# Optimization experiments

Measured on AMD Instinct MI355X. Metric: run time of the kernel, lower is better.

The kernel has to match this reference:

```python
import jax, jax.numpy as jnp
import numpy as np

B, S, D = 4, 2048, 256
H = 8
KD = D  # keras MHA key_dim = input_shape[-1] -> per-head dim equals D
EPS = 1e-5


def layer_norm(x, gamma, beta):
    mu = jnp.mean(x, axis=-1, keepdims=True)
    var = jnp.var(x, axis=-1, keepdims=True)
    return (x - mu) * jax.lax.rsqrt(var + EPS) * gamma + beta


def setup_inputs() -> dict:
    key = jax.random.key(0)
    ks = jax.random.split(key, 12)
    scale = 1.0 / np.sqrt(D)
    inp = {
        "input_query": jax.random.normal(ks[0], (B, S, D), jnp.float32),
        "key": jax.random.normal(ks[1], (B, S, D), jnp.float32),
        "value": jax.random.normal(ks[2], (B, S, D), jnp.float32),
        # LayerNorm params (3 separate norms)
        "gq": jnp.ones((D,), jnp.float32), "bq_ln": jnp.zeros((D,), jnp.float32),
        "gk": jnp.ones((D,), jnp.float32), "bk_ln": jnp.zeros((D,), jnp.float32),
        "gv": jnp.ones((D,), jnp.float32), "bv_ln": jnp.zeros((D,), jnp.float32),
        # MHA projection weights: [D, H, KD] for q/k/v, [H, KD, D] for output
        "Wq": jax.random.normal(ks[3], (D, H, KD), jnp.float32) * scale,
        "bq": jnp.zeros((H, KD), jnp.float32),
        "Wk": jax.random.normal(ks[4], (D, H, KD), jnp.float32) * scale,
        "bk": jnp.zeros((H, KD), jnp.float32),
        "Wv": jax.random.normal(ks[5], (D, H, KD), jnp.float32) * scale,
        "bv": jnp.zeros((H, KD), jnp.float32),
        "Wo": jax.random.normal(ks[6], (H, KD, D), jnp.float32) * scale,
        "bo": jnp.zeros((D,), jnp.float32),
    }
    return inp


def reference(input_query, key, value, gq, bq_ln, gk, bk_ln, gv, bv_ln,
              Wq, bq, Wk, bk, Wv, bv, Wo, bo):
    # pre-LN on each stream
    q_in = layer_norm(input_query, gq, bq_ln)
    k_in = layer_norm(key, gk, bk_ln)
    v_in = layer_norm(value, gv, bv_ln)

    # projections -> [B, S, H, KD]
    q = jnp.einsum('bsd,dhk->bshk', q_in, Wq) + bq
    k = jnp.einsum('bsd,dhk->bshk', k_in, Wk) + bk
    v = jnp.einsum('bsd,dhk->bshk', v_in, Wv) + bv

    # scaled dot-product attention (keras scales query by 1/sqrt(key_dim))
    q = q * (1.0 / np.sqrt(KD)).astype(np.float32)
    scores = jnp.einsum('bqhk,bshk->bhqs', q, k)  # [B, H, Sq, Sk]
    probs = jax.nn.softmax(scores, axis=-1)
    # dropout = 0.0 (inference)
    attn = jnp.einsum('bhqs,bshk->bqhk', probs, v)
    out = jnp.einsum('bqhk,hkd->bqd', attn, Wo) + bo

    return input_query + out
```

## Files before the change

### kernel.cpp

```cpp
#include <hip/hip_runtime.h>

using bf16x8 = __attribute__((ext_vector_type(8))) __bf16;
using f32x4  = __attribute__((ext_vector_type(4))) float;
using f32x16 = __attribute__((ext_vector_type(16))) float;
typedef unsigned short u16;
typedef const __attribute__((address_space(1))) void* gas_p;
typedef __attribute__((address_space(3))) void* las_p;

__device__ __forceinline__ u16 f2bf(float f) {
  union { float f; unsigned u; } v; v.f = f;
  unsigned r = v.u + 0x7fffu + ((v.u >> 16) & 1u);
  return (u16)(r >> 16);
}

__device__ __forceinline__ unsigned pkbf(float a, float b) {
  unsigned r;
  asm("v_cvt_pk_bf16_f32 %0, %1, %2" : "=v"(r) : "v"(a), "v"(b));
  return r;
}

__device__ __forceinline__ void gload16(const void* g, void* l) {
  __builtin_amdgcn_global_load_lds((gas_p)g, (las_p)l, 16, 0, 0);
}

#define MFMA(a, b, c)   __builtin_amdgcn_mfma_f32_16x16x32_bf16((a), (b), (c), 0, 0, 0)
#define MFMA32(a, b, c) __builtin_amdgcn_mfma_f32_32x32x16_bf16((a), (b), (c), 0, 0, 0)

__global__ __launch_bounds__(256) void transpose_conv(
    const float* __restrict__ Wq, const float* __restrict__ Wk,
    const float* __restrict__ Wv, const float* __restrict__ Wo,
    u16* __restrict__ wqt, u16* __restrict__ wkt,
    u16* __restrict__ wvt, u16* __restrict__ wot)
{
  int z = blockIdx.y;
  const float* src = (z == 0) ? Wq : (z == 1) ? Wk : (z == 2) ? Wv : Wo;
  u16* dst = (z == 0) ? wqt : (z == 1) ? wkt : (z == 2) ? wvt : wot;
  int C = (z < 3) ? 2048 : 256;
  int R = (z < 3) ? 256 : 2048;
  int TC = C >> 5;
  int tc = blockIdx.x % TC, tr = blockIdx.x / TC;
  __shared__ float tile[32][33];
  int j = threadIdx.x & 31, i0 = threadIdx.x >> 5;
#pragma unroll
  for (int p = 0; p < 4; p++)
    tile[i0 + p * 8][j] = src[(tr * 32 + i0 + p * 8) * C + tc * 32 + j];
  __syncthreads();
#pragma unroll
  for (int p = 0; p < 4; p++)
    dst[(tc * 32 + i0 + p * 8) * R + tr * 32 + j] = f2bf(tile[j][i0 + p * 8]);
}

__global__ __launch_bounds__(256) void ln3_kernel(
    const float* __restrict__ xq, const float* __restrict__ xk, const float* __restrict__ xv,
    const float* __restrict__ gq, const float* __restrict__ bq,
    const float* __restrict__ gk, const float* __restrict__ bk,
    const float* __restrict__ gv, const float* __restrict__ bv,
    u16* __restrict__ oq, u16* __restrict__ ok, u16* __restrict__ ov)
{
  int z = blockIdx.y;
  const float* x = (z == 0) ? xq : (z == 1) ? xk : xv;
  const float* g = (z == 0) ? gq : (z == 1) ? gk : gv;
  const float* be = (z == 0) ? bq : (z == 1) ? bk : bv;
  u16* o = (z == 0) ? oq : (z == 1) ? ok : ov;
  int w = threadIdx.x >> 6, l = threadIdx.x & 63;
  int row = blockIdx.x * 4 + w;
  float4 x4 = *(const float4*)(x + row * 256 + l * 4);
  float s = x4.x + x4.y + x4.z + x4.w;
  float sq = x4.x * x4.x + x4.y * x4.y + x4.z * x4.z + x4.w * x4.w;
#pragma unroll
  for (int mm = 1; mm < 64; mm <<= 1) { s += __shfl_xor(s, mm); sq += __shfl_xor(sq, mm); }
  float mu = s * (1.f / 256.f);
  float var = sq * (1.f / 256.f) - mu * mu;
  float rs = rsqrtf(var + 1e-5f);
  float4 g4 = *(const float4*)(g + l * 4);
  float4 b4 = *(const float4*)(be + l * 4);
  ushort4 o4;
  o4.x = f2bf((x4.x - mu) * rs * g4.x + b4.x);
  o4.y = f2bf((x4.y - mu) * rs * g4.y + b4.y);
  o4.z = f2bf((x4.z - mu) * rs * g4.z + b4.z);
  o4.w = f2bf((x4.w - mu) * rs * g4.w + b4.w);
  *(ushort4*)(o + row * 256 + l * 4) = o4;
}

__global__ __launch_bounds__(256) void proj_gemm(
    const u16* __restrict__ qn, const u16* __restrict__ kn, const u16* __restrict__ vn,
    const u16* __restrict__ wqt, const u16* __restrict__ wkt, const u16* __restrict__ wvt,
    const float* __restrict__ bq, const float* __restrict__ bk, const float* __restrict__ bv,
    u16* __restrict__ qo, u16* __restrict__ ko, u16* __restrict__ vo)
{
  __shared__ u16 As[128 * 64];
  __shared__ u16 Bs[128 * 64];
  int z = blockIdx.z;
  const u16* A  = (z == 0) ? qn : (z == 1) ? kn : vn;
  const u16* Bt = (z == 0) ? wqt : (z == 1) ? wkt : wvt;
  const float* bias = (z == 0) ? bq : (z == 1) ? bk : bv;
  u16* Co = (z == 0) ? qo : (z == 1) ? ko : vo;
  float scale = (z == 0) ? 0.0625f : 1.0f;

  int i0 = blockIdx.x * 128, n0 = blockIdx.y * 128;
  int tid = threadIdx.x, w = tid >> 6, l = tid & 63;
  int wr = w >> 1, wc = w & 1, l15 = l & 15, qv = l >> 4;

  f32x4 acc[4][4] = {};

  for (int k0 = 0; k0 < 256; k0 += 64) {
    __syncthreads();
#pragma unroll
    for (int j = 0; j < 4; j++) {
      int c = (w * 4 + j) * 64 + l;
      int row = c >> 3, co = (c & 7) * 8;
      gload16(A + (i0 + row) * 256 + k0 + co, (char*)As + (w * 4 + j) * 1024);
      gload16(Bt + (n0 + row) * 256 + k0 + co, (char*)Bs + (w * 4 + j) * 1024);
    }
    __syncthreads();
#pragma unroll
    for (int kk = 0; kk < 2; kk++) {
      bf16x8 a[4], bfr[4];
#pragma unroll
      for (int m = 0; m < 4; m++)
        a[m] = *(const bf16x8*)(As + (wr * 64 + m * 16 + l15) * 64 + kk * 32 + qv * 8);
#pragma unroll
      for (int n = 0; n < 4; n++)
        bfr[n] = *(const bf16x8*)(Bs + (wc * 64 + n * 16 + l15) * 64 + kk * 32 + qv * 8);
#pragma unroll
      for (int m = 0; m < 4; m++)
#pragma unroll
        for (int n = 0; n < 4; n++) acc[m][n] = MFMA(a[m], bfr[n], acc[m][n]);
    }
  }

  if (z == 2) {
#pragma unroll
    for (int n = 0; n < 4; n++) {
      int col = n0 + wc * 64 + n * 16 + l15;
      float bc = bias[col];
      int h = col >> 8, kd = col & 255;
#pragma unroll
      for (int m = 0; m < 4; m++) {
        int row0 = i0 + wr * 64 + m * 16 + qv * 4;
        int bb = row0 >> 11, ss = row0 & 2047;
        ushort4 o4;
        o4.x = f2bf(acc[m][n][0] + bc);
        o4.y = f2bf(acc[m][n][1] + bc);
        o4.z = f2bf(acc[m][n][2] + bc);
        o4.w = f2bf(acc[m][n][3] + bc);
        *(ushort4*)(Co + ((size_t)(bb * 8 + h) * 256 + kd) * 2048 + ss) = o4;
      }
    }
  } else {
#pragma unroll
    for (int n = 0; n < 4; n++) {
      int col = n0 + wc * 64 + n * 16 + l15;
      float bc = bias[col];
      int h = col >> 8, kd = col & 255;
#pragma unroll
      for (int m = 0; m < 4; m++) {
#pragma unroll
        for (int r = 0; r < 4; r++) {
          int row = i0 + wr * 64 + m * 16 + qv * 4 + r;
          int bb = row >> 11, ss = row & 2047;
          Co[((bb * 8 + h) * 2048 + ss) * 256 + kd] = f2bf((acc[m][n][r] + bc) * scale);
        }
      }
    }
  }
}

__global__ __launch_bounds__(512, 2) void flash_attn(
    const u16* __restrict__ q, const u16* __restrict__ k,
    const u16* __restrict__ vt, u16* __restrict__ o)
{
  __shared__ char lds[131072];
  int f = blockIdx.x;
  int qt = f >> 5;
  int bh = (f & 7) | (((f >> 3) & 3) << 3);
  int b = bh >> 3, hh = bh & 7;
  int tid = threadIdx.x, w = tid >> 6, l = tid & 63;
  int l31 = l & 31, h = l >> 5;

  const u16* Q = q + (size_t)(bh * 2048 + qt * 256 + w * 32) * 256;
  const u16* K = k + (size_t)bh * 2048 * 256;
  const u16* V = vt + (size_t)bh * 256 * 2048;

  bf16x8 qf[16];
#pragma unroll
  for (int dt = 0; dt < 16; dt++)
    qf[dt] = *(const bf16x8*)(Q + l31 * 256 + dt * 16 + h * 8);

  f32x16 oacc[8] = {};
  float m_ = -1e30f, lsum = 0.f;

  auto stage = [&](int t, char* base) {
#pragma unroll
    for (int j = 0; j < 4; j++) {
      int c = w * 4 + j;
      int off = c * 1024 + l * 16;
      {
        int r = off >> 9, ps = l & 31;
        gload16(K + (size_t)(t * 64 + r) * 256 + ((ps ^ (r & 31)) << 3), base + off);
      }
      {
        int r = off >> 8, ps = l & 15;
        int lsl = ps ^ (r & 15);
        int d = r * 2 + (lsl >> 3);
        gload16(V + (size_t)d * 2048 + t * 64 + ((lsl & 7) << 3), base + 32768 + off);
      }
    }
  };

  stage(0, lds);
  __syncthreads();

  for (int t = 0; t < 32; t++) {
    char* cur = lds + (size_t)(t & 1) * 65536;
    char* nxt = lds + (size_t)((t + 1) & 1) * 65536;
    if (t + 1 < 32) stage(t + 1, nxt);

    f32x16 p0 = {}, p1 = {};
    __builtin_amdgcn_s_setprio(1);
#pragma unroll
    for (int dt = 0; dt < 16; dt++) {
      int sl = ((dt * 2 + h) ^ l31) << 4;
      bf16x8 kf0 = *(const bf16x8*)(cur + l31 * 512 + sl);
      bf16x8 kf1 = *(const bf16x8*)(cur + (32 + l31) * 512 + sl);
      p0 = MFMA32(kf0, qf[dt], p0);
      p1 = MFMA32(kf1, qf[dt], p1);
    }
    __builtin_amdgcn_s_setprio(0);

    float n0 = fmaxf(fmaxf(p0[0], p0[1]), fmaxf(p0[2], p0[3]));
    float n1 = fmaxf(fmaxf(p0[4], p0[5]), fmaxf(p0[6], p0[7]));
    float n2 = fmaxf(fmaxf(p0[8], p0[9]), fmaxf(p0[10], p0[11]));
    float n3 = fmaxf(fmaxf(p0[12], p0[13]), fmaxf(p0[14], p0[15]));
    float n4 = fmaxf(fmaxf(p1[0], p1[1]), fmaxf(p1[2], p1[3]));
    float n5 = fmaxf(fmaxf(p1[4], p1[5]), fmaxf(p1[6], p1[7]));
    float n6 = fmaxf(fmaxf(p1[8], p1[9]), fmaxf(p1[10], p1[11]));
    float n7 = fmaxf(fmaxf(p1[12], p1[13]), fmaxf(p1[14], p1[15]));
    float mt = fmaxf(fmaxf(fmaxf(n0, n1), fmaxf(n2, n3)),
                     fmaxf(fmaxf(n4, n5), fmaxf(n6, n7)));
    mt = fmaxf(mt, __shfl_xor(mt, 32));
    if (__any(mt > m_ + 8.0f)) {
      float mn = fmaxf(m_, mt);
      float fsc = __expf(m_ - mn);
      lsum *= fsc;
#pragma unroll
      for (int dt = 0; dt < 8; dt++)
#pragma unroll
        for (int i = 0; i < 16; i++) oacc[dt][i] *= fsc;
      m_ = mn;
    }
#pragma unroll
    for (int i = 0; i < 16; i++) { p0[i] = __expf(p0[i] - m_); lsum += p0[i]; }
#pragma unroll
    for (int i = 0; i < 16; i++) { p1[i] = __expf(p1[i] - m_); lsum += p1[i]; }

    unsigned pw[16];
#pragma unroll
    for (int i = 0; i < 8; i++) pw[i] = pkbf(p0[2 * i], p0[2 * i + 1]);
#pragma unroll
    for (int i = 0; i < 8; i++) pw[8 + i] = pkbf(p1[2 * i], p1[2 * i + 1]);

#pragma unroll
    for (int kt = 0; kt < 4; kt++) {
      unsigned x0 = __shfl_xor(pw[4 * kt + 0], 32);
      unsigned x1 = __shfl_xor(pw[4 * kt + 1], 32);
      unsigned x2 = __shfl_xor(pw[4 * kt + 2], 32);
      unsigned x3 = __shfl_xor(pw[4 * kt + 3], 32);
      union { unsigned u[4]; bf16x8 v; } pa;
      pa.u[0] = h ? x2 : pw[4 * kt + 0];
      pa.u[1] = h ? x3 : pw[4 * kt + 1];
      pa.u[2] = h ? pw[4 * kt + 2] : x0;
      pa.u[3] = h ? pw[4 * kt + 3] : x1;
      __builtin_amdgcn_s_setprio(1);
#pragma unroll
      for (int dt = 0; dt < 8; dt++) {
        int d = dt * 32 + l31;
        int r = d >> 1;
        int lsl = (d & 1) * 8 + kt * 2 + h;
        bf16x8 vf = *(const bf16x8*)(cur + 32768 + r * 256 + ((lsl ^ (r & 15)) << 4));
        oacc[dt] = MFMA32(vf, pa.v, oacc[dt]);
      }
      __builtin_amdgcn_s_setprio(0);
    }

    asm volatile("s_waitcnt vmcnt(0)" ::: "memory");
    __syncthreads();
  }

  __syncthreads();
  float inv = 1.0f / (lsum + __shfl_xor(lsum, 32));
  char* wbase = (char*)lds + w * 8192;
  int qr15 = l31 & 15;
#pragma unroll
  for (int ph = 0; ph < 2; ph++) {
    if ((l31 >> 4) == ph) {
#pragma unroll
      for (int dt = 0; dt < 8; dt++) {
#pragma unroll
        for (int rg = 0; rg < 4; rg++) {
          uint2 uu;
          uu.x = pkbf(oacc[dt][rg * 4 + 0] * inv, oacc[dt][rg * 4 + 1] * inv);
          uu.y = pkbf(oacc[dt][rg * 4 + 2] * inv, oacc[dt][rg * 4 + 3] * inv);
          *(uint2*)(wbase + qr15 * 512 + ((dt * 64 + rg * 16) ^ (qr15 << 4)) + h * 8) = uu;
        }
      }
    }
    asm volatile("s_waitcnt lgkmcnt(0)" ::: "memory");
    __builtin_amdgcn_sched_barrier(0);
#pragma unroll
    for (int c = 0; c < 8; c++) {
      int qr = c * 2 + h;
      uint4 vv = *(const uint4*)(wbase + qr * 512 + ((l31 ^ qr) << 4));
      int s = qt * 256 + w * 32 + ph * 16 + qr;
      *(uint4*)((char*)o + (size_t)(b * 2048 + s) * 4096 + hh * 512 + l31 * 16) = vv;
    }
    asm volatile("s_waitcnt lgkmcnt(0)" ::: "memory");
  }
}

__global__ __launch_bounds__(256) void out_gemm(
    const u16* __restrict__ A, const u16* __restrict__ Bt,
    const float* __restrict__ bo, const float* __restrict__ resid,
    float* __restrict__ out)
{
  __shared__ u16 As[128 * 64];
  __shared__ u16 Bs[64 * 64];
  int i0 = blockIdx.x * 128, n0 = blockIdx.y * 64;
  int tid = threadIdx.x, w = tid >> 6, l = tid & 63, l15 = l & 15, qv = l >> 4;

  f32x4 acc[2][4] = {};

  for (int k0 = 0; k0 < 2048; k0 += 64) {
    __syncthreads();
#pragma unroll
    for (int j = 0; j < 4; j++) {
      int c = (w * 4 + j) * 64 + l;
      int row = c >> 3, co = (c & 7) * 8;
      gload16(A + (i0 + row) * 2048 + k0 + co, (char*)As + (w * 4 + j) * 1024);
    }
#pragma unroll
    for (int j = 0; j < 2; j++) {
      int c = (w * 2 + j) * 64 + l;
      int row = c >> 3, co = (c & 7) * 8;
      gload16(Bt + (n0 + row) * 2048 + k0 + co, (char*)Bs + (w * 2 + j) * 1024);
    }
    __syncthreads();
#pragma unroll
    for (int kk = 0; kk < 2; kk++) {
      bf16x8 a[2], bfr[4];
#pragma unroll
      for (int m = 0; m < 2; m++)
        a[m] = *(const bf16x8*)(As + (w * 32 + m * 16 + l15) * 64 + kk * 32 + qv * 8);
#pragma unroll
      for (int n = 0; n < 4; n++)
        bfr[n] = *(const bf16x8*)(Bs + (n * 16 + l15) * 64 + kk * 32 + qv * 8);
#pragma unroll
      for (int m = 0; m < 2; m++)
#pragma unroll
        for (int n = 0; n < 4; n++) acc[m][n] = MFMA(a[m], bfr[n], acc[m][n]);
    }
  }

#pragma unroll
  for (int n = 0; n < 4; n++) {
    int col = n0 + n * 16 + l15;
    float bc = bo[col];
#pragma unroll
    for (int m = 0; m < 2; m++)
#pragma unroll
      for (int r = 0; r < 4; r++) {
        int row = i0 + w * 32 + m * 16 + qv * 4 + r;
        out[row * 256 + col] = acc[m][n][r] + bc + resid[row * 256 + col];
      }
  }
}

extern "C" void kernel_launch(void* const* d_in, const int* in_sizes, int n_in,
                              void* d_out, int out_size, void* d_ws, size_t ws_size,
                              hipStream_t stream)
{
  const float* inq  = (const float*)d_in[0];
  const float* key  = (const float*)d_in[1];
  const float* val  = (const float*)d_in[2];
  const float* gq   = (const float*)d_in[3];
  const float* bqln = (const float*)d_in[4];
  const float* gk   = (const float*)d_in[5];
  const float* bkln = (const float*)d_in[6];
  const float* gv   = (const float*)d_in[7];
  const float* bvln = (const float*)d_in[8];
  const float* Wq   = (const float*)d_in[9];
  const float* bq   = (const float*)d_in[10];
  const float* Wk   = (const float*)d_in[11];
  const float* bk   = (const float*)d_in[12];
  const float* Wv   = (const float*)d_in[13];
  const float* bv   = (const float*)d_in[14];
  const float* Wo   = (const float*)d_in[15];
  const float* bo   = (const float*)d_in[16];

  char* ws = (char*)d_ws;
  const size_t MB = 1ull << 20;
  u16* wqt = (u16*)(ws + 0 * MB);
  u16* wkt = (u16*)(ws + 1 * MB);
  u16* wvt = (u16*)(ws + 2 * MB);
  u16* wot = (u16*)(ws + 3 * MB);
  u16* qn  = (u16*)(ws + 4 * MB);
  u16* kn  = (u16*)(ws + 8 * MB);
  u16* vn  = (u16*)(ws + 12 * MB);
  u16* qws = (u16*)(ws + 16 * MB);
  u16* kws = (u16*)(ws + 48 * MB);
  u16* attn = (u16*)(ws + 80 * MB);
  u16* vtw = (u16*)(ws + 112 * MB);

  transpose_conv<<<dim3(512, 4), 256, 0, stream>>>(Wq, Wk, Wv, Wo, wqt, wkt, wvt, wot);
  ln3_kernel<<<dim3(2048, 3), 256, 0, stream>>>(inq, key, val, gq, bqln, gk, bkln, gv, bvln,
                                                qn, kn, vn);
  proj_gemm<<<dim3(64, 16, 3), 256, 0, stream>>>(qn, kn, vn, wqt, wkt, wvt, bq, bk, bv,
                                                 qws, kws, vtw);
  flash_attn<<<256, 512, 0, stream>>>(qws, kws, vtw, attn);
  out_gemm<<<dim3(64, 4), 256, 0, stream>>>(attn, wot, bo, inq, (float*)d_out);
}
```

Baseline: 267.3 us.

## Shrink flash-attention tiles to 128 queries and 32-key blocks with 4 waves

Flash attention now uses 256-thread blocks covering 128 query rows (down from 512 threads and 256 rows) and streams K/V in 32-key tiles instead of 64-key tiles. LDS drops from 128KB to 64KB and the grid doubles to 512 blocks, with a new block-to-(batch,head,qtile) mapping. The aim is more blocks and higher occupancy across the CUs. The cost is twice as many loop iterations, each with its own barrier and staging overhead, and less K/V reuse per block. The swizzled LDS layouts for K and V are reworked to match the new tile sizes, and the redundant barrier before the epilogue is removed.

```diff
diff --git a/kernel.cpp b/kernel.cpp
--- a/kernel.cpp
+++ b/kernel.cpp
@@ -166,19 +166,20 @@
   }
 }
 
-__global__ __launch_bounds__(512, 2) void flash_attn(
+__global__ __launch_bounds__(256, 2) void flash_attn(
     const u16* __restrict__ q, const u16* __restrict__ k,
     const u16* __restrict__ vt, u16* __restrict__ o)
 {
-  __shared__ char lds[131072];
+  __shared__ char lds[65536];
   int f = blockIdx.x;
-  int qt = f >> 5;
-  int bh = (f & 7) | (((f >> 3) & 3) << 3);
+  int slot = f >> 3;
+  int bh = (f & 7) * 4 + (slot & 3);
+  int qt = slot >> 2;
   int b = bh >> 3, hh = bh & 7;
   int tid = threadIdx.x, w = tid >> 6, l = tid & 63;
   int l31 = l & 31, h = l >> 5;
 
-  const u16* Q = q + (size_t)(bh * 2048 + qt * 256 + w * 32) * 256;
+  const u16* Q = q + (size_t)(bh * 2048 + qt * 128 + w * 32) * 256;
   const u16* K = k + (size_t)bh * 2048 * 256;
   const u16* V = vt + (size_t)bh * 256 * 2048;
 
@@ -196,14 +197,14 @@
       int c = w * 4 + j;
       int off = c * 1024 + l * 16;
       {
-        int r = off >> 9, ps = l & 31;
-        gload16(K + (size_t)(t * 64 + r) * 256 + ((ps ^ (r & 31)) << 3), base + off);
+        int r = off >> 9, ps = (off >> 4) & 31;
+        gload16(K + (size_t)(t * 32 + r) * 256 + ((ps ^ r) << 3), base + off);
       }
       {
-        int r = off >> 8, ps = l & 15;
-        int lsl = ps ^ (r & 15);
-        int d = r * 2 + (lsl >> 3);
-        gload16(V + (size_t)d * 2048 + t * 64 + ((lsl & 7) << 3), base + 32768 + off);
+        int r = off >> 8, g = (off >> 4) & 15;
+        int gg = g ^ (r & 15);
+        int d = r * 4 + (gg >> 2), s0 = (gg & 3) * 8;
+        gload16(V + (size_t)d * 2048 + t * 32 + s0, base + 16384 + off);
       }
     }
   };
@@ -211,33 +212,25 @@
   stage(0, lds);
   __syncthreads();
 
-  for (int t = 0; t < 32; t++) {
-    char* cur = lds + (size_t)(t & 1) * 65536;
-    char* nxt = lds + (size_t)((t + 1) & 1) * 65536;
-    if (t + 1 < 32) stage(t + 1, nxt);
-
-    f32x16 p0 = {}, p1 = {};
+  for (int t = 0; t < 64; t++) {
+    char* cur = lds + (size_t)(t & 1) * 32768;
+    char* nxt = lds + (size_t)((t + 1) & 1) * 32768;
+    if (t + 1 < 64) stage(t + 1, nxt);
+
+    f32x16 p = {};
     __builtin_amdgcn_s_setprio(1);
 #pragma unroll
     for (int dt = 0; dt < 16; dt++) {
-      int sl = ((dt * 2 + h) ^ l31) << 4;
-      bf16x8 kf0 = *(const bf16x8*)(cur + l31 * 512 + sl);
-      bf16x8 kf1 = *(const bf16x8*)(cur + (32 + l31) * 512 + sl);
-      p0 = MFMA32(kf0, qf[dt], p0);
-      p1 = MFMA32(kf1, qf[dt], p1);
+      bf16x8 kf = *(const bf16x8*)(cur + l31 * 512 + (((dt * 2 + h) ^ l31) << 4));
+      p = MFMA32(kf, qf[dt], p);
     }
     __builtin_amdgcn_s_setprio(0);
 
-    float n0 = fmaxf(fmaxf(p0[0], p0[1]), fmaxf(p0[2], p0[3]));
-    float n1 = fmaxf(fmaxf(p0[4], p0[5]), fmaxf(p0[6], p0[7]));
-    float n2 = fmaxf(fmaxf(p0[8], p0[9]), fmaxf(p0[10], p0[11]));
-    float n3 = fmaxf(fmaxf(p0[12], p0[13]), fmaxf(p0[14], p0[15]));
-    float n4 = fmaxf(fmaxf(p1[0], p1[1]), fmaxf(p1[2], p1[3]));
-    float n5 = fmaxf(fmaxf(p1[4], p1[5]), fmaxf(p1[6], p1[7]));
-    float n6 = fmaxf(fmaxf(p1[8], p1[9]), fmaxf(p1[10], p1[11]));
-    float n7 = fmaxf(fmaxf(p1[12], p1[13]), fmaxf(p1[14], p1[15]));
-    float mt = fmaxf(fmaxf(fmaxf(n0, n1), fmaxf(n2, n3)),
-                     fmaxf(fmaxf(n4, n5), fmaxf(n6, n7)));
+    float n0 = fmaxf(fmaxf(p[0], p[1]), fmaxf(p[2], p[3]));
+    float n1 = fmaxf(fmaxf(p[4], p[5]), fmaxf(p[6], p[7]));
+    float n2 = fmaxf(fmaxf(p[8], p[9]), fmaxf(p[10], p[11]));
+    float n3 = fmaxf(fmaxf(p[12], p[13]), fmaxf(p[14], p[15]));
+    float mt = fmaxf(fmaxf(n0, n1), fmaxf(n2, n3));
     mt = fmaxf(mt, __shfl_xor(mt, 32));
     if (__any(mt > m_ + 8.0f)) {
       float mn = fmaxf(m_, mt);
@@ -250,18 +243,14 @@
       m_ = mn;
     }
 #pragma unroll
-    for (int i = 0; i < 16; i++) { p0[i] = __expf(p0[i] - m_); lsum += p0[i]; }
-#pragma unroll
-    for (int i = 0; i < 16; i++) { p1[i] = __expf(p1[i] - m_); lsum += p1[i]; }
-
-    unsigned pw[16];
-#pragma unroll
-    for (int i = 0; i < 8; i++) pw[i] = pkbf(p0[2 * i], p0[2 * i + 1]);
-#pragma unroll
-    for (int i = 0; i < 8; i++) pw[8 + i] = pkbf(p1[2 * i], p1[2 * i + 1]);
-
-#pragma unroll
-    for (int kt = 0; kt < 4; kt++) {
+    for (int i = 0; i < 16; i++) { p[i] = __expf(p[i] - m_); lsum += p[i]; }
+
+    unsigned pw[8];
+#pragma unroll
+    for (int i = 0; i < 8; i++) pw[i] = pkbf(p[2 * i], p[2 * i + 1]);
+
+#pragma unroll
+    for (int kt = 0; kt < 2; kt++) {
       unsigned x0 = __shfl_xor(pw[4 * kt + 0], 32);
       unsigned x1 = __shfl_xor(pw[4 * kt + 1], 32);
       unsigned x2 = __shfl_xor(pw[4 * kt + 2], 32);
@@ -275,9 +264,9 @@
 #pragma unroll
       for (int dt = 0; dt < 8; dt++) {
         int d = dt * 32 + l31;
-        int r = d >> 1;
-        int lsl = (d & 1) * 8 + kt * 2 + h;
-        bf16x8 vf = *(const bf16x8*)(cur + 32768 + r * 256 + ((lsl ^ (r & 15)) << 4));
+        int r = d >> 2;
+        int gg = (d & 3) * 4 + kt * 2 + h;
+        bf16x8 vf = *(const bf16x8*)(cur + 16384 + r * 256 + ((gg ^ (r & 15)) << 4));
         oacc[dt] = MFMA32(vf, pa.v, oacc[dt]);
       }
       __builtin_amdgcn_s_setprio(0);
@@ -287,7 +276,6 @@
     __syncthreads();
   }
 
-  __syncthreads();
   float inv = 1.0f / (lsum + __shfl_xor(lsum, 32));
   char* wbase = (char*)lds + w * 8192;
   int qr15 = l31 & 15;
@@ -311,7 +299,7 @@
     for (int c = 0; c < 8; c++) {
       int qr = c * 2 + h;
       uint4 vv = *(const uint4*)(wbase + qr * 512 + ((l31 ^ qr) << 4));
-      int s = qt * 256 + w * 32 + ph * 16 + qr;
+      int s = qt * 128 + w * 32 + ph * 16 + qr;
       *(uint4*)((char*)o + (size_t)(b * 2048 + s) * 4096 + hh * 512 + l31 * 16) = vv;
     }
     asm volatile("s_waitcnt lgkmcnt(0)" ::: "memory");
@@ -416,6 +404,6 @@
                                                 qn, kn, vn);
   proj_gemm<<<dim3(64, 16, 3), 256, 0, stream>>>(qn, kn, vn, wqt, wkt, wvt, bq, bk, bv,
                                                  qws, kws, vtw);
-  flash_attn<<<256, 512, 0, stream>>>(qws, kws, vtw, attn);
+  flash_attn<<<512, 256, 0, stream>>>(qws, kws, vtw, attn);
   out_gemm<<<dim3(64, 4), 256, 0, stream>>>(attn, wot, bo, inq, (float*)d_out);
 }
```

Measured after the change: 313.1 us. 17.2% more time.

## Split attention tile into halves and use exp2 with log2e-folded query scale

Applied to the files above, without the earlier changes.

Folds log2(e) into the query projection scale so softmax can use the native v_exp_f32 (exp2) instead of __expf, dropping a multiply per element. The 64-key tile is also processed as two 32-key halves: QK for the first half, then its softmax and PV, then the second half, so softmax VALU work can interleave with the other half's MFMAs. The running max can now be rescaled twice per tile, which may add rescale work. The threshold for lazy rescaling is scaled to match the new log2 domain.

```diff
diff --git a/kernel.cpp b/kernel.cpp
--- a/kernel.cpp
+++ b/kernel.cpp
@@ -7,6 +7,8 @@
 typedef const __attribute__((address_space(1))) void* gas_p;
 typedef __attribute__((address_space(3))) void* las_p;
 
+#define LOG2E 1.4426950408889634f
+
 __device__ __forceinline__ u16 f2bf(float f) {
   union { float f; unsigned u; } v; v.f = f;
   unsigned r = v.u + 0x7fffu + ((v.u >> 16) & 1u);
@@ -16,6 +18,12 @@
 __device__ __forceinline__ unsigned pkbf(float a, float b) {
   unsigned r;
   asm("v_cvt_pk_bf16_f32 %0, %1, %2" : "=v"(r) : "v"(a), "v"(b));
+  return r;
+}
+
+__device__ __forceinline__ float exp2v(float x) {
+  float r;
+  asm("v_exp_f32 %0, %1" : "=v"(r) : "v"(x));
   return r;
 }
 
@@ -95,7 +103,7 @@
   const u16* Bt = (z == 0) ? wqt : (z == 1) ? wkt : wvt;
   const float* bias = (z == 0) ? bq : (z == 1) ? bk : bv;
   u16* Co = (z == 0) ? qo : (z == 1) ? ko : vo;
-  float scale = (z == 0) ? 0.0625f : 1.0f;
+  float scale = (z == 0) ? 0.0625f * LOG2E : 1.0f;
 
   int i0 = blockIdx.x * 128, n0 = blockIdx.y * 128;
   int tid = threadIdx.x, w = tid >> 6, l = tid & 63;
@@ -208,40 +216,16 @@
     }
   };
 
-  stage(0, lds);
-  __syncthreads();
-
-  for (int t = 0; t < 32; t++) {
-    char* cur = lds + (size_t)(t & 1) * 65536;
-    char* nxt = lds + (size_t)((t + 1) & 1) * 65536;
-    if (t + 1 < 32) stage(t + 1, nxt);
-
-    f32x16 p0 = {}, p1 = {};
-    __builtin_amdgcn_s_setprio(1);
-#pragma unroll
-    for (int dt = 0; dt < 16; dt++) {
-      int sl = ((dt * 2 + h) ^ l31) << 4;
-      bf16x8 kf0 = *(const bf16x8*)(cur + l31 * 512 + sl);
-      bf16x8 kf1 = *(const bf16x8*)(cur + (32 + l31) * 512 + sl);
-      p0 = MFMA32(kf0, qf[dt], p0);
-      p1 = MFMA32(kf1, qf[dt], p1);
-    }
-    __builtin_amdgcn_s_setprio(0);
-
-    float n0 = fmaxf(fmaxf(p0[0], p0[1]), fmaxf(p0[2], p0[3]));
-    float n1 = fmaxf(fmaxf(p0[4], p0[5]), fmaxf(p0[6], p0[7]));
-    float n2 = fmaxf(fmaxf(p0[8], p0[9]), fmaxf(p0[10], p0[11]));
-    float n3 = fmaxf(fmaxf(p0[12], p0[13]), fmaxf(p0[14], p0[15]));
-    float n4 = fmaxf(fmaxf(p1[0], p1[1]), fmaxf(p1[2], p1[3]));
-    float n5 = fmaxf(fmaxf(p1[4], p1[5]), fmaxf(p1[6], p1[7]));
-    float n6 = fmaxf(fmaxf(p1[8], p1[9]), fmaxf(p1[10], p1[11]));
-    float n7 = fmaxf(fmaxf(p1[12], p1[13]), fmaxf(p1[14], p1[15]));
-    float mt = fmaxf(fmaxf(fmaxf(n0, n1), fmaxf(n2, n3)),
-                     fmaxf(fmaxf(n4, n5), fmaxf(n6, n7)));
+  auto softmax_half = [&](f32x16& p, unsigned* pw) {
+    float n0 = fmaxf(fmaxf(p[0], p[1]), fmaxf(p[2], p[3]));
+    float n1 = fmaxf(fmaxf(p[4], p[5]), fmaxf(p[6], p[7]));
+    float n2 = fmaxf(fmaxf(p[8], p[9]), fmaxf(p[10], p[11]));
+    float n3 = fmaxf(fmaxf(p[12], p[13]), fmaxf(p[14], p[15]));
+    float mt = fmaxf(fmaxf(n0, n1), fmaxf(n2, n3));
     mt = fmaxf(mt, __shfl_xor(mt, 32));
-    if (__any(mt > m_ + 8.0f)) {
+    if (__any(mt > m_ + 8.0f * LOG2E)) {
       float mn = fmaxf(m_, mt);
-      float fsc = __expf(m_ - mn);
+      float fsc = exp2v(m_ - mn);
       lsum *= fsc;
 #pragma unroll
       for (int dt = 0; dt < 8; dt++)
@@ -250,27 +234,24 @@
       m_ = mn;
     }
 #pragma unroll
-    for (int i = 0; i < 16; i++) { p0[i] = __expf(p0[i] - m_); lsum += p0[i]; }
-#pragma unroll
-    for (int i = 0; i < 16; i++) { p1[i] = __expf(p1[i] - m_); lsum += p1[i]; }
-
-    unsigned pw[16];
-#pragma unroll
-    for (int i = 0; i < 8; i++) pw[i] = pkbf(p0[2 * i], p0[2 * i + 1]);
-#pragma unroll
-    for (int i = 0; i < 8; i++) pw[8 + i] = pkbf(p1[2 * i], p1[2 * i + 1]);
-
-#pragma unroll
-    for (int kt = 0; kt < 4; kt++) {
-      unsigned x0 = __shfl_xor(pw[4 * kt + 0], 32);
-      unsigned x1 = __shfl_xor(pw[4 * kt + 1], 32);
-      unsigned x2 = __shfl_xor(pw[4 * kt + 2], 32);
-      unsigned x3 = __shfl_xor(pw[4 * kt + 3], 32);
+    for (int i = 0; i < 16; i++) { p[i] = exp2v(p[i] - m_); lsum += p[i]; }
+#pragma unroll
+    for (int i = 0; i < 8; i++) pw[i] = pkbf(p[2 * i], p[2 * i + 1]);
+  };
+
+  auto pv_half = [&](const unsigned* pw, int hf, const char* cur) {
+#pragma unroll
+    for (int ktl = 0; ktl < 2; ktl++) {
+      int kt = hf * 2 + ktl;
+      unsigned x0 = __shfl_xor(pw[4 * ktl + 0], 32);
+      unsigned x1 = __shfl_xor(pw[4 * ktl + 1], 32);
+      unsigned x2 = __shfl_xor(pw[4 * ktl + 2], 32);
+      unsigned x3 = __shfl_xor(pw[4 * ktl + 3], 32);
       union { unsigned u[4]; bf16x8 v; } pa;
-      pa.u[0] = h ? x2 : pw[4 * kt + 0];
-      pa.u[1] = h ? x3 : pw[4 * kt + 1];
-      pa.u[2] = h ? pw[4 * kt + 2] : x0;
-      pa.u[3] = h ? pw[4 * kt + 3] : x1;
+      pa.u[0] = h ? x2 : pw[4 * ktl + 0];
+      pa.u[1] = h ? x3 : pw[4 * ktl + 1];
+      pa.u[2] = h ? pw[4 * ktl + 2] : x0;
+      pa.u[3] = h ? pw[4 * ktl + 3] : x1;
       __builtin_amdgcn_s_setprio(1);
 #pragma unroll
       for (int dt = 0; dt < 8; dt++) {
@@ -282,6 +263,37 @@
       }
       __builtin_amdgcn_s_setprio(0);
     }
+  };
+
+  stage(0, lds);
+  __syncthreads();
+
+  for (int t = 0; t < 32; t++) {
+    char* cur = lds + (size_t)(t & 1) * 65536;
+    char* nxt = lds + (size_t)((t + 1) & 1) * 65536;
+    if (t + 1 < 32) stage(t + 1, nxt);
+
+    f32x16 p0 = {}, p1 = {};
+    unsigned pw0[8], pw1[8];
+    __builtin_amdgcn_s_setprio(1);
+#pragma unroll
+    for (int dt = 0; dt < 16; dt++) {
+      int sl = ((dt * 2 + h) ^ l31) << 4;
+      bf16x8 kf0 = *(const bf16x8*)(cur + l31 * 512 + sl);
+      p0 = MFMA32(kf0, qf[dt], p0);
+    }
+#pragma unroll
+    for (int dt = 0; dt < 16; dt++) {
+      int sl = ((dt * 2 + h) ^ l31) << 4;
+      bf16x8 kf1 = *(const bf16x8*)(cur + (32 + l31) * 512 + sl);
+      p1 = MFMA32(kf1, qf[dt], p1);
+    }
+    __builtin_amdgcn_s_setprio(0);
+
+    softmax_half(p0, pw0);
+    pv_half(pw0, 0, cur);
+    softmax_half(p1, pw1);
+    pv_half(pw1, 1, cur);
 
     asm volatile("s_waitcnt vmcnt(0)" ::: "memory");
     __syncthreads();
```

New measurement: 334.6 us. 1.25x slower.

## Use FP8 for P·V in flash attention with exp2 softmax

Applied to the files above, without the earlier changes.

The V projection is now written as FP8 in a permuted layout, and the attention probabilities are packed to FP8, so the P·V product uses 32x32x16 fp8 MFMAs instead of bf16. This halves V staging traffic and the LDS footprint. Log2e is folded into the Q scale so the softmax can use raw v_exp_f32, and permlane32_swap replaces the xor-32 shuffles. Precision drops noticeably for both P and V, and the rescale threshold is tightened.

```diff
diff --git a/kernel.cpp b/kernel.cpp
--- a/kernel.cpp
+++ b/kernel.cpp
@@ -3,9 +3,12 @@
 using bf16x8 = __attribute__((ext_vector_type(8))) __bf16;
 using f32x4  = __attribute__((ext_vector_type(4))) float;
 using f32x16 = __attribute__((ext_vector_type(16))) float;
+using uint2v = __attribute__((ext_vector_type(2))) unsigned;
 typedef unsigned short u16;
 typedef const __attribute__((address_space(1))) void* gas_p;
 typedef __attribute__((address_space(3))) void* las_p;
+
+#define LOG2E 1.4426950408889634f
 
 __device__ __forceinline__ u16 f2bf(float f) {
   union { float f; unsigned u; } v; v.f = f;
@@ -19,12 +22,29 @@
   return r;
 }
 
+__device__ __forceinline__ float exp2v(float x) {
+  float r;
+  asm("v_exp_f32 %0, %1" : "=v"(r) : "v"(x));
+  return r;
+}
+
+__device__ __forceinline__ unsigned pk_fp8x4(float a, float b, float c, float d) {
+  int w = __builtin_amdgcn_cvt_pk_fp8_f32(a, b, 0, false);
+  w = __builtin_amdgcn_cvt_pk_fp8_f32(c, d, w, true);
+  return (unsigned)w;
+}
+
+__device__ __forceinline__ uint2v swap32(unsigned a, unsigned b) {
+  return __builtin_amdgcn_permlane32_swap(a, b, false, false);
+}
+
 __device__ __forceinline__ void gload16(const void* g, void* l) {
   __builtin_amdgcn_global_load_lds((gas_p)g, (las_p)l, 16, 0, 0);
 }
 
 #define MFMA(a, b, c)   __builtin_amdgcn_mfma_f32_16x16x32_bf16((a), (b), (c), 0, 0, 0)
 #define MFMA32(a, b, c) __builtin_amdgcn_mfma_f32_32x32x16_bf16((a), (b), (c), 0, 0, 0)
+#define MFMA8(a, b, c)  __builtin_amdgcn_mfma_f32_32x32x16_fp8_fp8((a), (b), (c), 0, 0, 0)
 
 __global__ __launch_bounds__(256) void transpose_conv(
     const float* __restrict__ Wq, const float* __restrict__ Wk,
@@ -86,7 +106,7 @@
     const u16* __restrict__ qn, const u16* __restrict__ kn, const u16* __restrict__ vn,
     const u16* __restrict__ wqt, const u16* __restrict__ wkt, const u16* __restrict__ wvt,
     const float* __restrict__ bq, const float* __restrict__ bk, const float* __restrict__ bv,
-    u16* __restrict__ qo, u16* __restrict__ ko, u16* __restrict__ vo)
+    u16* __restrict__ qo, u16* __restrict__ ko, unsigned char* __restrict__ vo)
 {
   __shared__ u16 As[128 * 64];
   __shared__ u16 Bs[128 * 64];
@@ -94,8 +114,7 @@
   const u16* A  = (z == 0) ? qn : (z == 1) ? kn : vn;
   const u16* Bt = (z == 0) ? wqt : (z == 1) ? wkt : wvt;
   const float* bias = (z == 0) ? bq : (z == 1) ? bk : bv;
-  u16* Co = (z == 0) ? qo : (z == 1) ? ko : vo;
-  float scale = (z == 0) ? 0.0625f : 1.0f;
+  float scale = (z == 0) ? 0.0625f * LOG2E : 1.0f;
 
   int i0 = blockIdx.x * 128, n0 = blockIdx.y * 128;
   int tid = threadIdx.x, w = tid >> 6, l = tid & 63;
@@ -134,32 +153,31 @@
     for (int n = 0; n < 4; n++) {
       int col = n0 + wc * 64 + n * 16 + l15;
       float bc = bias[col];
-      int h = col >> 8, kd = col & 255;
+      int hd = col >> 8, kd = col & 255;
 #pragma unroll
       for (int m = 0; m < 4; m++) {
         int row0 = i0 + wr * 64 + m * 16 + qv * 4;
         int bb = row0 >> 11, ss = row0 & 2047;
-        ushort4 o4;
-        o4.x = f2bf(acc[m][n][0] + bc);
-        o4.y = f2bf(acc[m][n][1] + bc);
-        o4.z = f2bf(acc[m][n][2] + bc);
-        o4.w = f2bf(acc[m][n][3] + bc);
-        *(ushort4*)(Co + ((size_t)(bb * 8 + h) * 256 + kd) * 2048 + ss) = o4;
+        unsigned wv = pk_fp8x4(acc[m][n][0] + bc, acc[m][n][1] + bc,
+                               acc[m][n][2] + bc, acc[m][n][3] + bc);
+        int pos = (ss & ~63) | (((ss >> 3) & 3) << 4) | (((ss >> 5) & 1) << 3) | (ss & 7);
+        *(unsigned*)(vo + ((size_t)(bb * 8 + hd) * 256 + kd) * 2048 + pos) = wv;
       }
     }
   } else {
+    u16* Co = (z == 0) ? qo : ko;
 #pragma unroll
     for (int n = 0; n < 4; n++) {
       int col = n0 + wc * 64 + n * 16 + l15;
       float bc = bias[col];
-      int h = col >> 8, kd = col & 255;
+      int hd = col >> 8, kd = col & 255;
 #pragma unroll
       for (int m = 0; m < 4; m++) {
 #pragma unroll
         for (int r = 0; r < 4; r++) {
           int row = i0 + wr * 64 + m * 16 + qv * 4 + r;
           int bb = row >> 11, ss = row & 2047;
-          Co[((bb * 8 + h) * 2048 + ss) * 256 + kd] = f2bf((acc[m][n][r] + bc) * scale);
+          Co[((bb * 8 + hd) * 2048 + ss) * 256 + kd] = f2bf((acc[m][n][r] + bc) * scale);
         }
       }
     }
@@ -168,9 +186,9 @@
 
 __global__ __launch_bounds__(512, 2) void flash_attn(
     const u16* __restrict__ q, const u16* __restrict__ k,
-    const u16* __restrict__ vt, u16* __restrict__ o)
-{
-  __shared__ char lds[131072];
+    const unsigned char* __restrict__ vt, u16* __restrict__ o)
+{
+  __shared__ char lds[98304];
   int f = blockIdx.x;
   int qt = f >> 5;
   int bh = (f & 7) | (((f >> 3) & 3) << 3);
@@ -180,7 +198,7 @@
 
   const u16* Q = q + (size_t)(bh * 2048 + qt * 256 + w * 32) * 256;
   const u16* K = k + (size_t)bh * 2048 * 256;
-  const u16* V = vt + (size_t)bh * 256 * 2048;
+  const unsigned char* V = vt + (size_t)bh * 256 * 2048;
 
   bf16x8 qf[16];
 #pragma unroll
@@ -195,16 +213,17 @@
     for (int j = 0; j < 4; j++) {
       int c = w * 4 + j;
       int off = c * 1024 + l * 16;
-      {
-        int r = off >> 9, ps = l & 31;
-        gload16(K + (size_t)(t * 64 + r) * 256 + ((ps ^ (r & 31)) << 3), base + off);
-      }
-      {
-        int r = off >> 8, ps = l & 15;
-        int lsl = ps ^ (r & 15);
-        int d = r * 2 + (lsl >> 3);
-        gload16(V + (size_t)d * 2048 + t * 64 + ((lsl & 7) << 3), base + 32768 + off);
-      }
+      int r = off >> 9, ps = l & 31;
+      gload16(K + (size_t)(t * 64 + r) * 256 + ((ps ^ (r & 31)) << 3), base + off);
+    }
+#pragma unroll
+    for (int j = 0; j < 2; j++) {
+      int c = w * 2 + j;
+      int off = c * 1024 + l * 16;
+      int r = off >> 8, pg = (off >> 4) & 15;
+      int g = pg ^ (r & 15);
+      int d = r + 64 * (g >> 2), sc = g & 3;
+      gload16(V + (size_t)d * 2048 + t * 64 + sc * 16, base + 32768 + off);
     }
   };
 
@@ -212,8 +231,8 @@
   __syncthreads();
 
   for (int t = 0; t < 32; t++) {
-    char* cur = lds + (size_t)(t & 1) * 65536;
-    char* nxt = lds + (size_t)((t + 1) & 1) * 65536;
+    char* cur = lds + (size_t)(t & 1) * 49152;
+    char* nxt = lds + (size_t)((t + 1) & 1) * 49152;
     if (t + 1 < 32) stage(t + 1, nxt);
 
     f32x16 p0 = {}, p1 = {};
@@ -238,10 +257,13 @@
     float n7 = fmaxf(fmaxf(p1[12], p1[13]), fmaxf(p1[14], p1[15]));
     float mt = fmaxf(fmaxf(fmaxf(n0, n1), fmaxf(n2, n3)),
                      fmaxf(fmaxf(n4, n5), fmaxf(n6, n7)));
-    mt = fmaxf(mt, __shfl_xor(mt, 32));
-    if (__any(mt > m_ + 8.0f)) {
+    {
+      uint2v mr = swap32(__builtin_bit_cast(unsigned, mt), __builtin_bit_cast(unsigned, mt));
+      mt = fmaxf(__builtin_bit_cast(float, mr.x), __builtin_bit_cast(float, mr.y));
+    }
+    if (__any(mt > m_ + 7.0f)) {
       float mn = fmaxf(m_, mt);
-      float fsc = __expf(m_ - mn);
+      float fsc = exp2v(m_ - mn);
       lsum *= fsc;
 #pragma unroll
       for (int dt = 0; dt < 8; dt++)
@@ -250,35 +272,33 @@
       m_ = mn;
     }
 #pragma unroll
-    for (int i = 0; i < 16; i++) { p0[i] = __expf(p0[i] - m_); lsum += p0[i]; }
-#pragma unroll
-    for (int i = 0; i < 16; i++) { p1[i] = __expf(p1[i] - m_); lsum += p1[i]; }
-
-    unsigned pw[16];
-#pragma unroll
-    for (int i = 0; i < 8; i++) pw[i] = pkbf(p0[2 * i], p0[2 * i + 1]);
-#pragma unroll
-    for (int i = 0; i < 8; i++) pw[8 + i] = pkbf(p1[2 * i], p1[2 * i + 1]);
-
-#pragma unroll
-    for (int kt = 0; kt < 4; kt++) {
-      unsigned x0 = __shfl_xor(pw[4 * kt + 0], 32);
-      unsigned x1 = __shfl_xor(pw[4 * kt + 1], 32);
-      unsigned x2 = __shfl_xor(pw[4 * kt + 2], 32);
-      unsigned x3 = __shfl_xor(pw[4 * kt + 3], 32);
-      union { unsigned u[4]; bf16x8 v; } pa;
-      pa.u[0] = h ? x2 : pw[4 * kt + 0];
-      pa.u[1] = h ? x3 : pw[4 * kt + 1];
-      pa.u[2] = h ? pw[4 * kt + 2] : x0;
-      pa.u[3] = h ? pw[4 * kt + 3] : x1;
+    for (int i = 0; i < 16; i++) { p0[i] = exp2v(p0[i] - m_); lsum += p0[i]; }
+#pragma unroll
+    for (int i = 0; i < 16; i++) { p1[i] = exp2v(p1[i] - m_); lsum += p1[i]; }
+
+    unsigned pwf0[4], pwf1[4];
+#pragma unroll
+    for (int j = 0; j < 4; j++) {
+      pwf0[j] = pk_fp8x4(p0[4 * j], p0[4 * j + 1], p0[4 * j + 2], p0[4 * j + 3]);
+      pwf1[j] = pk_fp8x4(p1[4 * j], p1[4 * j + 1], p1[4 * j + 2], p1[4 * j + 3]);
+    }
+
+#pragma unroll
+    for (int k2 = 0; k2 < 2; k2++) {
+      uint2v f0 = swap32(pwf0[k2 * 2], pwf0[k2 * 2 + 1]);
+      uint2v f1 = swap32(pwf1[k2 * 2], pwf1[k2 * 2 + 1]);
+      long long pA = (long long)(((unsigned long long)f0.y << 32) | f0.x);
+      long long pB = (long long)(((unsigned long long)f1.y << 32) | f1.x);
       __builtin_amdgcn_s_setprio(1);
 #pragma unroll
       for (int dt = 0; dt < 8; dt++) {
-        int d = dt * 32 + l31;
-        int r = d >> 1;
-        int lsl = (d & 1) * 8 + kt * 2 + h;
-        bf16x8 vf = *(const bf16x8*)(cur + 32768 + r * 256 + ((lsl ^ (r & 15)) << 4));
-        oacc[dt] = MFMA32(vf, pa.v, oacc[dt]);
+        int r = (dt & 1) * 32 + l31;
+        int g = (dt >> 1) * 4 + k2 * 2 + h;
+        const uint4 vv = *(const uint4*)(cur + 32768 + r * 256 + ((g ^ (r & 15)) << 4));
+        long long vA = (long long)(((unsigned long long)vv.y << 32) | vv.x);
+        long long vB = (long long)(((unsigned long long)vv.w << 32) | vv.z);
+        oacc[dt] = MFMA8(vA, pA, oacc[dt]);
+        oacc[dt] = MFMA8(vB, pB, oacc[dt]);
       }
       __builtin_amdgcn_s_setprio(0);
     }
@@ -288,7 +308,12 @@
   }
 
   __syncthreads();
-  float inv = 1.0f / (lsum + __shfl_xor(lsum, 32));
+  float lsc;
+  {
+    uint2v lr = swap32(__builtin_bit_cast(unsigned, lsum), __builtin_bit_cast(unsigned, lsum));
+    lsc = __builtin_bit_cast(float, lr.x) + __builtin_bit_cast(float, lr.y);
+  }
+  float inv = 1.0f / lsc;
   char* wbase = (char*)lds + w * 8192;
   int qr15 = l31 & 15;
 #pragma unroll
@@ -409,7 +434,7 @@
   u16* qws = (u16*)(ws + 16 * MB);
   u16* kws = (u16*)(ws + 48 * MB);
   u16* attn = (u16*)(ws + 80 * MB);
-  u16* vtw = (u16*)(ws + 112 * MB);
+  unsigned char* vtw = (unsigned char*)(ws + 112 * MB);
 
   transpose_conv<<<dim3(512, 4), 256, 0, stream>>>(Wq, Wk, Wv, Wo, wqt, wkt, wvt, wot);
   ln3_kernel<<<dim3(2048, 3), 256, 0, stream>>>(inq, key, val, gq, bqln, gk, bkln, gv, bvln,
```

New measurement: 251.5 us. 5.9% less time.
